# Optimization experiments

Measured on AMD Instinct MI355X. Metric: run time of the kernel, lower is better.

Reference implementation:

```python
import jax, jax.numpy as jnp
import numpy as np

B, C, CI, H, W = 4, 64, 32, 64, 64
EPS = 1e-5

def _bn(x, p):
    # p: [4, C] = (gamma, beta, running_mean, running_var); eval-mode BatchNorm2d
    gamma, beta, mean, var = p
    inv = gamma / jnp.sqrt(var + EPS)
    return x * inv[None, :, None, None] + (beta - mean * inv)[None, :, None, None]

def _conv1x1(x, w, b):
    # x: (b, cin, h, w), w: (cout, cin), b: (cout,)
    return jnp.einsum('bchw,oc->bohw', x, w) + b[None, :, None, None]

def setup_inputs():
    key = jax.random.key(0)
    ks = jax.random.split(key, 10)
    def bn_p(k):
        kg, kb, km, kv = jax.random.split(k, 4)
        return jnp.stack([1.0 + 0.1 * jax.random.normal(kg, (C,)),
                          0.1 * jax.random.normal(kb, (C,)),
                          0.1 * jax.random.normal(km, (C,)),
                          0.5 + jax.random.uniform(kv, (C,))])
    return {
        'x1': jax.random.normal(ks[0], (B, C, H, W), dtype=jnp.float32),
        'x2': jax.random.normal(ks[1], (B, C, H, W), dtype=jnp.float32),
        'g_bn': bn_p(ks[2]),
        'g_w': 0.05 * jax.random.normal(ks[3], (CI, C)),
        'g_b': jnp.zeros((CI,), jnp.float32),
        'theta_bn': bn_p(ks[4]),
        'theta_w': 0.05 * jax.random.normal(ks[5], (CI, C)),
        'theta_b': jnp.zeros((CI,), jnp.float32),
        'phi_bn': bn_p(ks[6]),
        'phi_w': 0.05 * jax.random.normal(ks[7], (CI, C)),
        'phi_b': jnp.zeros((CI,), jnp.float32),
        'w_bn': bn_p(ks[8]),
        'W_w': 0.05 * jax.random.normal(ks[9], (C, CI)),
        'W_b': jnp.zeros((C,), jnp.float32),
    }

def reference(x1, x2, g_bn, g_w, g_b, theta_bn, theta_w, theta_b,
              phi_bn, phi_w, phi_b, w_bn, W_w, W_b):
    b = x1.shape[0]
    # shared 'g' projection applied to both frames
    g1 = _conv1x1(_bn(x1, g_bn), g_w, g_b).reshape(b, CI, -1)            # (b, Ci, N1)
    g2 = _conv1x1(_bn(x2, g_bn), g_w, g_b).reshape(b, CI, -1)            # (b, Ci, N2)
    th = _conv1x1(_bn(x1, theta_bn), theta_w, theta_b).reshape(b, CI, -1)  # (b, Ci, N1)
    ph = _conv1x1(_bn(x2, phi_bn), phi_w, phi_b).reshape(b, CI, -1)        # (b, Ci, N2)
    energy = jnp.einsum('bcn,bcm->bnm', th, ph)                          # (b, N1, N2)
    att2 = jax.nn.softmax(energy, axis=-2)  # softmax over N1 (dim=-2 of energy_space_1)
    att1 = jax.nn.softmax(energy, axis=-1)  # softmax over N2 (dim=-2 of energy_space_1^T)
    y1 = jnp.einsum('bcn,bnm->bcm', g1, att2).reshape(b, CI, *x2.shape[2:])
    y2 = jnp.einsum('bcm,bnm->bcn', g2, att1).reshape(b, CI, *x1.shape[2:])
    def w_out(y):
        return _bn(_conv1x1(y, W_w, W_b), w_bn)
    return (x1 + w_out(y1), x2 + w_out(y2))
```

## Files before the change

kernel.cpp:

```cpp
#include <hip/hip_runtime.h>
#include <hip/hip_bf16.h>
#include <cstdint>
#include <cstddef>


#define B_  4
#define C_  64
#define CI_ 32
#define N_  4096
static constexpr float EPS_   = 1e-5f;
static constexpr float LOG2E_ = 1.4426950408889634f;

typedef __attribute__((ext_vector_type(8))) short  short8;
typedef __attribute__((ext_vector_type(4))) short  short4v;
typedef __attribute__((ext_vector_type(4))) float  float4v;
typedef __attribute__((ext_vector_type(4))) __bf16 bf16x4;
typedef __attribute__((ext_vector_type(8))) __bf16 bf16x8;

__device__ __forceinline__ short f2bf(float f) {
    unsigned u = __float_as_uint(f);
    unsigned r = (u + 0x7fffu + ((u >> 16) & 1u)) >> 16;
    return (short)r;
}

__global__ __launch_bounds__(512) void proj_kernel(
    const float* __restrict__ x1, const float* __restrict__ x2,
    const float* __restrict__ g_w, const float* __restrict__ g_b, const float* __restrict__ g_bn,
    const float* __restrict__ t_w, const float* __restrict__ t_b, const float* __restrict__ t_bn,
    const float* __restrict__ p_w, const float* __restrict__ p_b, const float* __restrict__ p_bn,
    short* __restrict__ th_t, short* __restrict__ ph_t,
    short* __restrict__ g1l, short* __restrict__ g2l)
{
    const int side = blockIdx.x >> 8;
    const int rb   = blockIdx.x & 255;
    const int b    = rb >> 6;
    const int n0   = (rb & 63) * 64;
    const int tid  = threadIdx.x;
    const int wv   = tid >> 6, lane = tid & 63;
    const int lg   = lane >> 4, lr = lane & 15;

    const float* x   = side ? x2   : x1;
    const float* wA  = side ? p_w  : t_w;
    const float* bA  = side ? p_b  : t_b;
    const float* bnA = side ? p_bn : t_bn;
    short* outA      = side ? ph_t : th_t;
    short* outG      = side ? g2l  : g1l;
    const float scaleA = side ? 1.0f : LOG2E_;

    __shared__ short xs_t[64][72];
    __shared__ short wfb[2][32][72];
    __shared__ float bfold[2][CI_];

    for (int it = 0; it < 4; it++) {
        int idx = it * 512 + tid;
        int o = idx >> 6, c = idx & 63;
        float invA = bnA[c]  * rsqrtf(bnA[192 + c]  + EPS_);
        float invG = g_bn[c] * rsqrtf(g_bn[192 + c] + EPS_);
        wfb[0][o][c] = f2bf(wA[idx]  * invA * scaleA);
        wfb[1][o][c] = f2bf(g_w[idx] * invG);
    }
    if (tid < 2 * CI_) {
        int set = tid >> 5, o = tid & 31;
        const float* bn = set ? g_bn : bnA;
        const float* w  = set ? g_w  : wA;
        const float* bs = set ? g_b  : bA;
        float s = bs[o];
        for (int c = 0; c < C_; c++) {
            float inv = bn[c] * rsqrtf(bn[192 + c] + EPS_);
            s += w[o * C_ + c] * (bn[64 + c] - bn[128 + c] * inv);
        }
        bfold[set][o] = set ? s : s * scaleA;
    }
    const float* xb = x + (size_t)b * C_ * N_ + n0;
    for (int it = 0; it < 2; it++) {
        int idx = it * 512 + tid;
        int c = idx >> 4, nq = idx & 15;
        float4 xv = *(const float4*)(xb + (size_t)c * N_ + nq * 4);
        xs_t[nq * 4 + 0][c] = f2bf(xv.x);
        xs_t[nq * 4 + 1][c] = f2bf(xv.y);
        xs_t[nq * 4 + 2][c] = f2bf(xv.z);
        xs_t[nq * 4 + 3][c] = f2bf(xv.w);
    }
    __syncthreads();

    const int set = wv & 1;
    const int oT  = (wv >> 1) & 1;
    const int nP  = wv >> 2;

    const float4v zero4 = {0.f, 0.f, 0.f, 0.f};
    short8 wf0 = *(const short8*)&wfb[set][oT * 16 + lr][lg * 8];
    short8 wf1 = *(const short8*)&wfb[set][oT * 16 + lr][32 + lg * 8];
    float4v cinit = zero4;
#pragma unroll
    for (int i = 0; i < 4; ++i) cinit[i] = bfold[set][oT * 16 + lg * 4 + i];

#pragma unroll
    for (int t = 0; t < 2; ++t) {
        const int nT = nP * 2 + t;
        short8 xf0 = *(const short8*)&xs_t[nT * 16 + lr][lg * 8];
        short8 xf1 = *(const short8*)&xs_t[nT * 16 + lr][32 + lg * 8];
        float4v d = __builtin_amdgcn_mfma_f32_16x16x32_bf16(wf0, xf0, cinit, 0, 0, 0);
        d = __builtin_amdgcn_mfma_f32_16x16x32_bf16(wf1, xf1, d, 0, 0, 0);
        const int n = n0 + nT * 16 + lr;
        if (set == 0) {
            short4v v;
#pragma unroll
            for (int i = 0; i < 4; ++i) v[i] = f2bf(d[i]);
            *(short4v*)(outA + ((size_t)b * N_ + n) * CI_ + oT * 16 + lg * 4) = v;
        } else {
#pragma unroll
            for (int i = 0; i < 4; ++i)
                outG[((size_t)b * CI_ + oT * 16 + lg * 4 + i) * N_ + n] = f2bf(d[i]);
        }
    }
}

__global__ __launch_bounds__(512, 6) void apply_kernel(
    const short* __restrict__ th, const short* __restrict__ ph,
    const short* __restrict__ g1l, const short* __restrict__ g2l,
    const float* __restrict__ x1, const float* __restrict__ x2,
    const float* __restrict__ Ww, const float* __restrict__ Wb,
    const float* __restrict__ w_bn,
    float* __restrict__ out)
{
    const int bid  = blockIdx.x;
    const int grp  = bid & 7;
    const int side = grp >> 2;
    const int b    = grp & 3;
    const int r0   = (bid >> 3) * 64;
    const short* A  = side ? th : ph;
    const short* Bm = side ? ph : th;
    const short* V  = side ? g2l : g1l;
    const int tid = threadIdx.x;
    const int wv = tid >> 6, lane = tid & 63;
    const int cg = wv & 3, rg = wv >> 2;
    const int lg = lane >> 4, lr = lane & 15;

    __shared__ __align__(16) char smem[74752];
    short (*lb)[256][40] = (short(*)[256][40])smem;
    short (*lv)[32][264] = (short(*)[32][264])(smem + 40960);
    float (*buf2)[64][33] = (float(*)[64][33])smem;
    float (*sums)[64]     = (float(*)[64])(smem + 16896);
    float (*ybuf)[36]     = (float(*)[36])(smem + 17920);
    float (*wf2)[CI_]     = (float(*)[CI_])(smem + 27136);
    float *bf2v           = (float*)(smem + 35328);

    const short* Ab = A  + (size_t)b * N_ * CI_;
    const short* Bb = Bm + (size_t)b * N_ * CI_;
    const short* Vb = V  + (size_t)b * CI_ * N_;

    short8 afrag0 = *(const short8*)(Ab + (size_t)(r0 + rg * 32 + lr) * CI_ + lg * 8);
    short8 afrag1 = *(const short8*)(Ab + (size_t)(r0 + rg * 32 + 16 + lr) * CI_ + lg * 8);

    short8 ones8;
#pragma unroll
    for (int i = 0; i < 8; ++i) ones8[i] = (short)0x3F80;

    const float4v zero4 = {0.f, 0.f, 0.f, 0.f};
    float4v a00 = zero4, a01 = zero4;
    float4v a10 = zero4, a11 = zero4;
    float4v sum0 = zero4, sum1 = zero4;

    const int brow0 = tid >> 2,          bpart0 = tid & 3;
    const int brow1 = (512 + tid) >> 2,  bpart1 = (512 + tid) & 3;
    const int vrow0 = tid >> 5,          vpart0 = tid & 31;
    const int vrow1 = (512 + tid) >> 5,  vpart1 = (512 + tid) & 31;
    const short* gB0 = Bb + (size_t)brow0 * CI_ + bpart0 * 8;
    const short* gB1 = Bb + (size_t)brow1 * CI_ + bpart1 * 8;
    const short* gV0 = Vb + (size_t)vrow0 * N_ + vpart0 * 8;
    const short* gV1 = Vb + (size_t)vrow1 * N_ + vpart1 * 8;

    {
        short8 b0s = *(const short8*)gB0;
        short8 b1s = *(const short8*)gB1;
        short8 v0s = *(const short8*)gV0;
        short8 v1s = *(const short8*)gV1;
        *(short8*)&lb[0][brow0][bpart0 * 8] = b0s;
        *(short8*)&lb[0][brow1][bpart1 * 8] = b1s;
        *(short8*)&lv[0][vrow0][vpart0 * 8] = v0s;
        *(short8*)&lv[0][vrow1][vpart1 * 8] = v1s;
    }
    __syncthreads();

    int cur = 0;
    for (int win = 0; win < 16; ++win) {
        short8 bst0, bst1, vst0, vst1;
        if (win < 15) {
            const int s0n = (win + 1) * 256;
            bst0 = *(const short8*)(gB0 + (size_t)s0n * CI_);
            bst1 = *(const short8*)(gB1 + (size_t)s0n * CI_);
            vst0 = *(const short8*)(gV0 + s0n);
            vst1 = *(const short8*)(gV1 + s0n);
        }
        __builtin_amdgcn_s_setprio(1);
#pragma unroll
        for (int ch2 = 0; ch2 < 2; ++ch2) {
            const int c0 = ch2 * 128 + cg * 32;
            short8 b0 = *(const short8*)&lb[cur][c0 + lr][lg * 8];
            short8 b1 = *(const short8*)&lb[cur][c0 + 16 + lr][lg * 8];
            short4v v00 = *(const short4v*)&lv[cur][lr][c0 + lg * 4];
            short4v v01 = *(const short4v*)&lv[cur][lr][c0 + 16 + lg * 4];
            short4v v10 = *(const short4v*)&lv[cur][16 + lr][c0 + lg * 4];
            short4v v11 = *(const short4v*)&lv[cur][16 + lr][c0 + 16 + lg * 4];
            short8 vA0 = __builtin_shufflevector(v00, v01, 0, 1, 2, 3, 4, 5, 6, 7);
            short8 vA1 = __builtin_shufflevector(v10, v11, 0, 1, 2, 3, 4, 5, 6, 7);
            {
                float4v e0 = __builtin_amdgcn_mfma_f32_16x16x32_bf16(b0, afrag0, zero4, 0, 0, 0);
                float4v e1 = __builtin_amdgcn_mfma_f32_16x16x32_bf16(b1, afrag0, zero4, 0, 0, 0);
                float p0 = __builtin_amdgcn_exp2f(e0[0]), p1 = __builtin_amdgcn_exp2f(e0[1]);
                float p2 = __builtin_amdgcn_exp2f(e0[2]), p3 = __builtin_amdgcn_exp2f(e0[3]);
                float p4 = __builtin_amdgcn_exp2f(e1[0]), p5 = __builtin_amdgcn_exp2f(e1[1]);
                float p6 = __builtin_amdgcn_exp2f(e1[2]), p7 = __builtin_amdgcn_exp2f(e1[3]);
                bf16x8 q;
                q[0] = (__bf16)p0; q[1] = (__bf16)p1; q[2] = (__bf16)p2; q[3] = (__bf16)p3;
                q[4] = (__bf16)p4; q[5] = (__bf16)p5; q[6] = (__bf16)p6; q[7] = (__bf16)p7;
                short8 pk = __builtin_bit_cast(short8, q);
                a00  = __builtin_amdgcn_mfma_f32_16x16x32_bf16(vA0, pk, a00, 0, 0, 0);
                a01  = __builtin_amdgcn_mfma_f32_16x16x32_bf16(vA1, pk, a01, 0, 0, 0);
                sum0 = __builtin_amdgcn_mfma_f32_16x16x32_bf16(ones8, pk, sum0, 0, 0, 0);
            }
            {
                float4v e0 = __builtin_amdgcn_mfma_f32_16x16x32_bf16(b0, afrag1, zero4, 0, 0, 0);
                float4v e1 = __builtin_amdgcn_mfma_f32_16x16x32_bf16(b1, afrag1, zero4, 0, 0, 0);
                float p0 = __builtin_amdgcn_exp2f(e0[0]), p1 = __builtin_amdgcn_exp2f(e0[1]);
                float p2 = __builtin_amdgcn_exp2f(e0[2]), p3 = __builtin_amdgcn_exp2f(e0[3]);
                float p4 = __builtin_amdgcn_exp2f(e1[0]), p5 = __builtin_amdgcn_exp2f(e1[1]);
                float p6 = __builtin_amdgcn_exp2f(e1[2]), p7 = __builtin_amdgcn_exp2f(e1[3]);
                bf16x8 q;
                q[0] = (__bf16)p0; q[1] = (__bf16)p1; q[2] = (__bf16)p2; q[3] = (__bf16)p3;
                q[4] = (__bf16)p4; q[5] = (__bf16)p5; q[6] = (__bf16)p6; q[7] = (__bf16)p7;
                short8 pk = __builtin_bit_cast(short8, q);
                a10  = __builtin_amdgcn_mfma_f32_16x16x32_bf16(vA0, pk, a10, 0, 0, 0);
                a11  = __builtin_amdgcn_mfma_f32_16x16x32_bf16(vA1, pk, a11, 0, 0, 0);
                sum1 = __builtin_amdgcn_mfma_f32_16x16x32_bf16(ones8, pk, sum1, 0, 0, 0);
            }
        }
        __builtin_amdgcn_s_setprio(0);
        if (win < 15) {
            *(short8*)&lb[cur ^ 1][brow0][bpart0 * 8] = bst0;
            *(short8*)&lb[cur ^ 1][brow1][bpart1 * 8] = bst1;
            *(short8*)&lv[cur ^ 1][vrow0][vpart0 * 8] = vst0;
            *(short8*)&lv[cur ^ 1][vrow1][vpart1 * 8] = vst1;
        }
        __syncthreads();
        cur ^= 1;
    }

    const float s0r = sum0[0];
    const float s1r = sum1[0];

    if (cg >= 2) {
        float* r0p = buf2[cg - 2][rg * 32 + lr];
        float* r1p = buf2[cg - 2][rg * 32 + 16 + lr];
#pragma unroll
        for (int i = 0; i < 4; ++i) {
            r0p[4 * lg + i]      = a00[i];
            r0p[16 + 4 * lg + i] = a01[i];
            r1p[4 * lg + i]      = a10[i];
            r1p[16 + 4 * lg + i] = a11[i];
        }
    }
    if (lane < 16) {
        sums[cg][rg * 32 + lane]      = s0r;
        sums[cg][rg * 32 + 16 + lane] = s1r;
    }
    for (int i = tid; i < C_ * CI_; i += 512) {
        int co = i >> 5;
        float inv = w_bn[co] * rsqrtf(w_bn[192 + co] + EPS_);
        (&wf2[0][0])[i] = inv * Ww[i];
    }
    if (tid < C_) {
        float inv = w_bn[tid] * rsqrtf(w_bn[192 + tid] + EPS_);
        bf2v[tid] = inv * Wb[tid] + (w_bn[64 + tid] - w_bn[128 + tid] * inv);
    }
    __syncthreads();
    if (cg < 2) {
        float* r0p = buf2[cg][rg * 32 + lr];
        float* r1p = buf2[cg][rg * 32 + 16 + lr];
#pragma unroll
        for (int i = 0; i < 4; ++i) {
            r0p[4 * lg + i]      += a00[i];
            r0p[16 + 4 * lg + i] += a01[i];
            r1p[4 * lg + i]      += a10[i];
            r1p[16 + 4 * lg + i] += a11[i];
        }
    }
    __syncthreads();
    {
        int m = tid >> 3;
        int ci0 = (tid & 7) * 4;
        float s = (sums[0][m] + sums[1][m]) + (sums[2][m] + sums[3][m]);
        float inv = 1.0f / s;
#pragma unroll
        for (int q = 0; q < 4; ++q) {
            ybuf[m][ci0 + q] = (buf2[0][m][ci0 + q] + buf2[1][m][ci0 + q]) * inv;
        }
    }
    __syncthreads();

    const int m   = tid & 63;
    const int cog = tid >> 6;
    float4v yq[8];
#pragma unroll
    for (int q = 0; q < 8; ++q) yq[q] = *(const float4v*)&ybuf[m][q * 4];
    const float* xb2 = (side ? x2 : x1) + (size_t)b * C_ * N_;
    float* ob = out + (size_t)side * (B_ * C_ * N_) + (size_t)b * C_ * N_;
#pragma unroll
    for (int k = 0; k < 8; ++k) {
        const int co = cog * 8 + k;
        float a2 = bf2v[co];
#pragma unroll
        for (int ci = 0; ci < CI_; ++ci) a2 += wf2[co][ci] * yq[ci >> 2][ci & 3];
        ob[(size_t)co * N_ + r0 + m] = xb2[(size_t)co * N_ + r0 + m] + a2;
    }
}

extern "C" void kernel_launch(void* const* d_in, const int* in_sizes, int n_in,
                              void* d_out, int out_size, void* d_ws, size_t ws_size,
                              hipStream_t stream)
{
    (void)in_sizes; (void)n_in; (void)out_size; (void)ws_size;
    const float* x1   = (const float*)d_in[0];
    const float* x2   = (const float*)d_in[1];
    const float* g_bn = (const float*)d_in[2];
    const float* g_w  = (const float*)d_in[3];
    const float* g_b  = (const float*)d_in[4];
    const float* t_bn = (const float*)d_in[5];
    const float* t_w  = (const float*)d_in[6];
    const float* t_b  = (const float*)d_in[7];
    const float* p_bn = (const float*)d_in[8];
    const float* p_w  = (const float*)d_in[9];
    const float* p_b  = (const float*)d_in[10];
    const float* w_bn = (const float*)d_in[11];
    const float* W_w  = (const float*)d_in[12];
    const float* W_b  = (const float*)d_in[13];
    float* out = (float*)d_out;

    char* ws = (char*)d_ws;
    const size_t MB = 1u << 20;
    short* th_t = (short*)(ws + 0 * MB);
    short* ph_t = (short*)(ws + 1 * MB);
    short* g1l  = (short*)(ws + 2 * MB);
    short* g2l  = (short*)(ws + 3 * MB);

    proj_kernel<<<dim3(512), dim3(512), 0, stream>>>(
        x1, x2, g_w, g_b, g_bn, t_w, t_b, t_bn, p_w, p_b, p_bn,
        th_t, ph_t, g1l, g2l);

    apply_kernel<<<dim3(512), dim3(512), 0, stream>>>(
        th_t, ph_t, g1l, g2l, x1, x2, W_w, W_b, w_bn, out);
}
```

Measured before the change: 42.05 us.

## Load attention operands directly from global into MFMA fragments, dropping LDS staging

The projection kernel now writes the g values in a fragment-ready tiled layout: 32-column blocks of 1024 elements, permuted so each lane's 8 bf16 values are contiguous. The apply kernel then drops its double-buffered LDS staging of the B and V tiles and the per-window __syncthreads. Each wave instead loads its MFMA operands straight from global memory, relying on L2/cache reuse. This frees about 39KB of LDS and removes barriers, but exposes global-load latency directly in the inner loop with no explicit prefetch, and each wave now re-reads data that was previously shared through LDS.

```diff
diff --git a/kernel.cpp b/kernel.cpp
--- a/kernel.cpp
+++ b/kernel.cpp
@@ -14,7 +14,6 @@
 typedef __attribute__((ext_vector_type(8))) short  short8;
 typedef __attribute__((ext_vector_type(4))) short  short4v;
 typedef __attribute__((ext_vector_type(4))) float  float4v;
-typedef __attribute__((ext_vector_type(4))) __bf16 bf16x4;
 typedef __attribute__((ext_vector_type(8))) __bf16 bf16x8;
 
 __device__ __forceinline__ short f2bf(float f) {
@@ -29,7 +28,7 @@
     const float* __restrict__ t_w, const float* __restrict__ t_b, const float* __restrict__ t_bn,
     const float* __restrict__ p_w, const float* __restrict__ p_b, const float* __restrict__ p_bn,
     short* __restrict__ th_t, short* __restrict__ ph_t,
-    short* __restrict__ g1l, short* __restrict__ g2l)
+    short* __restrict__ g1q, short* __restrict__ g2q)
 {
     const int side = blockIdx.x >> 8;
     const int rb   = blockIdx.x & 255;
@@ -44,7 +43,7 @@
     const float* bA  = side ? p_b  : t_b;
     const float* bnA = side ? p_bn : t_bn;
     short* outA      = side ? ph_t : th_t;
-    short* outG      = side ? g2l  : g1l;
+    short* outG      = side ? g2q  : g1q;
     const float scaleA = side ? 1.0f : LOG2E_;
 
     __shared__ short xs_t[64][72];
@@ -108,16 +107,18 @@
             for (int i = 0; i < 4; ++i) v[i] = f2bf(d[i]);
             *(short4v*)(outA + ((size_t)b * N_ + n) * CI_ + oT * 16 + lg * 4) = v;
         } else {
+            const int pos = ((n >> 2) & 3) * 8 + ((n >> 4) & 1) * 4 + (n & 3);
+            short* vq = outG + (size_t)b * CI_ * N_ + (size_t)(n >> 5) * 1024 + pos;
 #pragma unroll
             for (int i = 0; i < 4; ++i)
-                outG[((size_t)b * CI_ + oT * 16 + lg * 4 + i) * N_ + n] = f2bf(d[i]);
+                vq[(oT * 16 + lg * 4 + i) * 32] = f2bf(d[i]);
         }
     }
 }
 
 __global__ __launch_bounds__(512, 6) void apply_kernel(
     const short* __restrict__ th, const short* __restrict__ ph,
-    const short* __restrict__ g1l, const short* __restrict__ g2l,
+    const short* __restrict__ g1q, const short* __restrict__ g2q,
     const float* __restrict__ x1, const float* __restrict__ x2,
     const float* __restrict__ Ww, const float* __restrict__ Wb,
     const float* __restrict__ w_bn,
@@ -130,15 +131,13 @@
     const int r0   = (bid >> 3) * 64;
     const short* A  = side ? th : ph;
     const short* Bm = side ? ph : th;
-    const short* V  = side ? g2l : g1l;
+    const short* V  = side ? g2q : g1q;
     const int tid = threadIdx.x;
     const int wv = tid >> 6, lane = tid & 63;
     const int cg = wv & 3, rg = wv >> 2;
     const int lg = lane >> 4, lr = lane & 15;
 
-    __shared__ __align__(16) char smem[74752];
-    short (*lb)[256][40] = (short(*)[256][40])smem;
-    short (*lv)[32][264] = (short(*)[32][264])(smem + 40960);
+    __shared__ __align__(16) char smem[35584];
     float (*buf2)[64][33] = (float(*)[64][33])smem;
     float (*sums)[64]     = (float(*)[64])(smem + 16896);
     float (*ybuf)[36]     = (float(*)[36])(smem + 17920);
@@ -161,49 +160,20 @@
     float4v a10 = zero4, a11 = zero4;
     float4v sum0 = zero4, sum1 = zero4;
 
-    const int brow0 = tid >> 2,          bpart0 = tid & 3;
-    const int brow1 = (512 + tid) >> 2,  bpart1 = (512 + tid) & 3;
-    const int vrow0 = tid >> 5,          vpart0 = tid & 31;
-    const int vrow1 = (512 + tid) >> 5,  vpart1 = (512 + tid) & 31;
-    const short* gB0 = Bb + (size_t)brow0 * CI_ + bpart0 * 8;
-    const short* gB1 = Bb + (size_t)brow1 * CI_ + bpart1 * 8;
-    const short* gV0 = Vb + (size_t)vrow0 * N_ + vpart0 * 8;
-    const short* gV1 = Vb + (size_t)vrow1 * N_ + vpart1 * 8;
-
-    {
-        short8 b0s = *(const short8*)gB0;
-        short8 b1s = *(const short8*)gB1;
-        short8 v0s = *(const short8*)gV0;
-        short8 v1s = *(const short8*)gV1;
-        *(short8*)&lb[0][brow0][bpart0 * 8] = b0s;
-        *(short8*)&lb[0][brow1][bpart1 * 8] = b1s;
-        *(short8*)&lv[0][vrow0][vpart0 * 8] = v0s;
-        *(short8*)&lv[0][vrow1][vpart1 * 8] = v1s;
-    }
-    __syncthreads();
-
-    int cur = 0;
+    const short* Bl0 = Bb + (size_t)lr * CI_ + lg * 8;
+    const short* Bl1 = Bb + (size_t)(16 + lr) * CI_ + lg * 8;
+    const short* Vl0 = Vb + (size_t)lr * 32 + lg * 8;
+    const short* Vl1 = Vb + (size_t)(16 + lr) * 32 + lg * 8;
+
     for (int win = 0; win < 16; ++win) {
-        short8 bst0, bst1, vst0, vst1;
-        if (win < 15) {
-            const int s0n = (win + 1) * 256;
-            bst0 = *(const short8*)(gB0 + (size_t)s0n * CI_);
-            bst1 = *(const short8*)(gB1 + (size_t)s0n * CI_);
-            vst0 = *(const short8*)(gV0 + s0n);
-            vst1 = *(const short8*)(gV1 + s0n);
-        }
-        __builtin_amdgcn_s_setprio(1);
 #pragma unroll
         for (int ch2 = 0; ch2 < 2; ++ch2) {
-            const int c0 = ch2 * 128 + cg * 32;
-            short8 b0 = *(const short8*)&lb[cur][c0 + lr][lg * 8];
-            short8 b1 = *(const short8*)&lb[cur][c0 + 16 + lr][lg * 8];
-            short4v v00 = *(const short4v*)&lv[cur][lr][c0 + lg * 4];
-            short4v v01 = *(const short4v*)&lv[cur][lr][c0 + 16 + lg * 4];
-            short4v v10 = *(const short4v*)&lv[cur][16 + lr][c0 + lg * 4];
-            short4v v11 = *(const short4v*)&lv[cur][16 + lr][c0 + 16 + lg * 4];
-            short8 vA0 = __builtin_shufflevector(v00, v01, 0, 1, 2, 3, 4, 5, 6, 7);
-            short8 vA1 = __builtin_shufflevector(v10, v11, 0, 1, 2, 3, 4, 5, 6, 7);
+            const int c = win * 256 + ch2 * 128 + cg * 32;
+            short8 b0  = *(const short8*)(Bl0 + (size_t)c * CI_);
+            short8 b1  = *(const short8*)(Bl1 + (size_t)c * CI_);
+            short8 vA0 = *(const short8*)(Vl0 + (size_t)(c >> 5) * 1024);
+            short8 vA1 = *(const short8*)(Vl1 + (size_t)(c >> 5) * 1024);
+            __builtin_amdgcn_s_setprio(1);
             {
                 float4v e0 = __builtin_amdgcn_mfma_f32_16x16x32_bf16(b0, afrag0, zero4, 0, 0, 0);
                 float4v e1 = __builtin_amdgcn_mfma_f32_16x16x32_bf16(b1, afrag0, zero4, 0, 0, 0);
@@ -234,21 +204,14 @@
                 a11  = __builtin_amdgcn_mfma_f32_16x16x32_bf16(vA1, pk, a11, 0, 0, 0);
                 sum1 = __builtin_amdgcn_mfma_f32_16x16x32_bf16(ones8, pk, sum1, 0, 0, 0);
             }
-        }
-        __builtin_amdgcn_s_setprio(0);
-        if (win < 15) {
-            *(short8*)&lb[cur ^ 1][brow0][bpart0 * 8] = bst0;
-            *(short8*)&lb[cur ^ 1][brow1][bpart1 * 8] = bst1;
-            *(short8*)&lv[cur ^ 1][vrow0][vpart0 * 8] = vst0;
-            *(short8*)&lv[cur ^ 1][vrow1][vpart1 * 8] = vst1;
-        }
-        __syncthreads();
-        cur ^= 1;
+            __builtin_amdgcn_s_setprio(0);
+        }
     }
 
     const float s0r = sum0[0];
     const float s1r = sum1[0];
 
+    __syncthreads();
     if (cg >= 2) {
         float* r0p = buf2[cg - 2][rg * 32 + lr];
         float* r1p = buf2[cg - 2][rg * 32 + 16 + lr];
@@ -340,13 +303,13 @@
     const size_t MB = 1u << 20;
     short* th_t = (short*)(ws + 0 * MB);
     short* ph_t = (short*)(ws + 1 * MB);
-    short* g1l  = (short*)(ws + 2 * MB);
-    short* g2l  = (short*)(ws + 3 * MB);
+    short* g1q  = (short*)(ws + 2 * MB);
+    short* g2q  = (short*)(ws + 3 * MB);
 
     proj_kernel<<<dim3(512), dim3(512), 0, stream>>>(
         x1, x2, g_w, g_b, g_bn, t_w, t_b, t_bn, p_w, p_b, p_bn,
-        th_t, ph_t, g1l, g2l);
+        th_t, ph_t, g1q, g2q);
 
     apply_kernel<<<dim3(512), dim3(512), 0, stream>>>(
-        th_t, ph_t, g1l, g2l, x1, x2, W_w, W_b, w_bn, out);
+        th_t, ph_t, g1q, g2q, x1, x2, W_w, W_b, w_bn, out);
 }
```

After: 48.03 us. 1.14x slower.
